# Kernel optimization log

Hardware: AMD Instinct MI355X
Metric: run time of the kernel (lower is better)

The kernel has to match this reference:

```python
import jax, jax.numpy as jnp
import numpy as np

N_NODES = 100000
N_EDGES = 800000
DIM = 300
N_GRAPHS = 64
ATOM_VOCAB = 41
WORD_VOCAB = 10000


def setup_inputs() -> dict:
    key = jax.random.key(0)
    ks = jax.random.split(key, 7)
    atoms = jax.random.randint(ks[0], (N_NODES,), 0, ATOM_VOCAB)
    words = jax.random.randint(ks[1], (N_NODES,), 0, WORD_VOCAB)
    x = jnp.stack([atoms, words], axis=-1)  # [N,2] int indices
    edge_index = jax.random.randint(ks[2], (2, N_EDGES), 0, N_NODES)
    batch = jnp.sort(jax.random.randint(ks[3], (N_NODES,), 0, N_GRAPHS))
    atom_table = jax.random.normal(ks[4], (ATOM_VOCAB, DIM), dtype=jnp.float32) * 0.02
    word_table = jax.random.normal(ks[5], (WORD_VOCAB, DIM), dtype=jnp.float32) * 0.02
    W = jax.random.normal(ks[6], (DIM, DIM), dtype=jnp.float32) / np.sqrt(DIM)
    b = jnp.zeros((DIM,), dtype=jnp.float32)
    return {"x": x, "edge_index": edge_index, "batch": batch,
            "atom_table": atom_table, "word_table": word_table,
            "W": W, "b": b, "num_hops": 3}


def reference(x, edge_index, batch, atom_table, word_table, W, b, num_hops):
    n = x.shape[0]
    # GCNConv: add self-loops, symmetric degree normalization
    loops = jnp.arange(n)
    src = jnp.concatenate([edge_index[0], loops])  # [E+N]
    dst = jnp.concatenate([edge_index[1], loops])
    deg = jax.ops.segment_sum(jnp.ones_like(dst, dtype=W.dtype), dst, num_segments=n)
    dinv = jnp.where(deg > 0, jax.lax.rsqrt(deg), 0.0)
    norm = dinv[src] * dinv[dst]  # [E+N]

    # embed_nodes: atom embedding + word embedding
    h = atom_table[x[:, 0]] + word_table[x[:, 1]]  # [N, D]

    # num_hops applications of the SAME GCNConv (shared W, b)
    for _ in range(num_hops):
        hw = h @ W  # [N, D]
        msg = hw[src] * norm[:, None]  # [E+N, D]
        h = jax.ops.segment_sum(msg, dst, num_segments=n) + b

    # global_mean_pool over batch assignment
    sums = jax.ops.segment_sum(h, batch, num_segments=N_GRAPHS)  # [G, D]
    cnt = jax.ops.segment_sum(jnp.ones((n,), h.dtype), batch, num_segments=N_GRAPHS)
    return sums / jnp.maximum(cnt, 1.0)[:, None]
```

## Files before the change

### kernel.cpp

```cpp
#include <hip/hip_runtime.h>
#include <hip/hip_fp16.h>

#define NG 64
#define NGRAPH_C 64
#define KPAD 10240

#define RSZ 12500
#define RSZP 6250
#define NC_MS 64

__device__ __forceinline__ unsigned f_as_u(float f) { union { float f; unsigned u; } c; c.f = f; return c.u; }
__device__ __forceinline__ float u_as_f(unsigned u) { union { unsigned u; float f; } c; c.u = u; return c.f; }

__device__ __forceinline__ int xcc_id() {
    unsigned x;
    asm volatile("s_getreg_b32 %0, hwreg(HW_REG_XCC_ID)" : "=s"(x));
    return (int)(x & 7u);
}

union H4 { uint2 u2; __half h[4]; };

__global__ __launch_bounds__(256) void k_mscount(const int* __restrict__ src, const int* __restrict__ dst,
                                                 unsigned* __restrict__ rep_in,
                                                 unsigned* __restrict__ rep_src,
                                                 int e, int n, int chunk, int npairs) {
    __shared__ unsigned hin[RSZP];
    __shared__ unsigned hsrc[RSZP];
    int c = blockIdx.x % NC_MS;
    int r = blockIdx.x / NC_MS;
    int base = r * RSZ;
    int t = threadIdx.x;
    for (int w = t; w < RSZP; w += 256) { hin[w] = 0u; hsrc[w] = 0u; }
    __syncthreads();
    int e0 = c * chunk, e1 = min(e, e0 + chunk);
    for (int i = e0 + t; i < e1; i += 256) {
        int s = src[i], d = dst[i];
        unsigned ud = (unsigned)(d - base);
        unsigned us = (unsigned)(s - base);
        if (ud < (unsigned)RSZ) atomicAdd(&hin[ud >> 1], 1u << ((ud & 1) * 16));
        if (us < (unsigned)RSZ) atomicAdd(&hsrc[us >> 1], 1u << ((us & 1) * 16));
    }
    __syncthreads();
    int lim = min(RSZ, n - base);
    if (lim <= 0) return;
    int plim = (lim + 1) >> 1;
    unsigned* gin  = rep_in  + (size_t)c * npairs + (base >> 1);
    unsigned* gsrc = rep_src + (size_t)c * npairs + (base >> 1);
    for (int w = t; w < plim; w += 256) { gin[w] = hin[w]; gsrc[w] = hsrc[w]; }
}

__global__ __launch_bounds__(256) void k_msreduce(const unsigned* __restrict__ rep_in,
                                                  unsigned* __restrict__ rep_src,
                                                  float* __restrict__ dinv,
                                                  unsigned* __restrict__ counts_src,
                                                  int n, int npairs) {
    int i2 = blockIdx.x * 256 + threadIdx.x;
    if (i2 >= npairs) return;
    unsigned slo = 0, shi = 0, rlo = 0, rhi = 0;
#pragma unroll 4
    for (int c = 0; c < NC_MS; ++c) {
        unsigned vi = rep_in[(size_t)c * npairs + i2];
        slo += vi & 0xFFFFu; shi += vi >> 16;
        unsigned vs = rep_src[(size_t)c * npairs + i2];
        rep_src[(size_t)c * npairs + i2] = rlo | (rhi << 16);
        rlo += vs & 0xFFFFu; rhi += vs >> 16;
    }
    int i = i2 * 2;
    dinv[i] = rsqrtf((float)(slo + 1u));
    counts_src[i] = rlo;
    if (i + 1 < n) {
        dinv[i + 1] = rsqrtf((float)(shi + 1u));
        counts_src[i + 1] = rhi;
    }
}

__global__ __launch_bounds__(256) void k_blocksum(const unsigned* __restrict__ counts,
                                                  unsigned* __restrict__ partials, int n) {
    __shared__ unsigned s[256];
    int base = blockIdx.x * 1024;
    unsigned sum = 0;
    for (int j = threadIdx.x; j < 1024; j += 256) {
        int i = base + j;
        sum += (i < n) ? counts[i] : 0u;
    }
    s[threadIdx.x] = sum;
    __syncthreads();
    for (int off = 128; off > 0; off >>= 1) {
        if (threadIdx.x < (unsigned)off) s[threadIdx.x] += s[threadIdx.x + off];
        __syncthreads();
    }
    if (threadIdx.x == 0) partials[blockIdx.x] = s[0];
}

__global__ __launch_bounds__(128) void k_scanpartials(unsigned* __restrict__ partials, int nb) {
    __shared__ unsigned s[128];
    int t = threadIdx.x;
    s[t] = (t < nb) ? partials[t] : 0u;
    __syncthreads();
    if (t == 0) {
        unsigned run = 0;
        for (int i = 0; i < nb; ++i) { unsigned v = s[i]; s[i] = run; run += v; }
    }
    __syncthreads();
    if (t < nb) partials[t] = s[t];
}

__global__ __launch_bounds__(256) void k_scanblock(const unsigned* __restrict__ counts,
                                                   const unsigned* __restrict__ partials,
                                                   unsigned* __restrict__ row_start, int n) {
    __shared__ unsigned s[256];
    int base = blockIdx.x * 1024;
    int t = threadIdx.x;
    unsigned v[4];
    unsigned tsum = 0;
#pragma unroll
    for (int j = 0; j < 4; ++j) {
        int i = base + t * 4 + j;
        v[j] = (i < n) ? counts[i] : 0u;
        tsum += v[j];
    }
    s[t] = tsum;
    __syncthreads();
    for (int off = 1; off < 256; off <<= 1) {
        unsigned x = (t >= off) ? s[t - off] : 0u;
        __syncthreads();
        s[t] += x;
        __syncthreads();
    }
    unsigned excl = (t > 0 ? s[t - 1] : 0u) + partials[blockIdx.x];
#pragma unroll
    for (int j = 0; j < 4; ++j) {
        int i = base + t * 4 + j;
        if (i < n) {
            row_start[i] = excl;
            excl += v[j];
            if (i == n - 1) row_start[n] = excl;
        }
    }
}

__global__ __launch_bounds__(256) void k_msfill(const int* __restrict__ src, const int* __restrict__ dst,
                                                const int* __restrict__ batch,
                                                const unsigned* __restrict__ row_start,
                                                const unsigned* __restrict__ pref,
                                                const float* __restrict__ dinv,
                                                uint2* __restrict__ euv,
                                                int e, int n, int chunk, int npairs) {
    __shared__ unsigned cur[RSZP];
    int c = blockIdx.x % NC_MS;
    int r = blockIdx.x / NC_MS;
    int base = r * RSZ;
    int t = threadIdx.x;
    for (int w = t; w < RSZP; w += 256) cur[w] = 0u;
    __syncthreads();
    int e0 = c * chunk, e1 = min(e, e0 + chunk);
    const unsigned* prefc = pref + (size_t)c * npairs;
    for (int i = e0 + t; i < e1; i += 256) {
        int s = src[i];
        unsigned us = (unsigned)(s - base);
        if (us < (unsigned)RSZ) {
            int d = dst[i];
            unsigned sh = (us & 1) * 16;
            unsigned old = atomicAdd(&cur[us >> 1], 1u << sh);
            unsigned slot = (old >> sh) & 0xFFFFu;
            unsigned p16 = (prefc[(unsigned)s >> 1] >> ((s & 1) * 16)) & 0xFFFFu;
            unsigned pos = row_start[s] + p16 + slot;
            uint2 pv;
            pv.x = (unsigned)d | ((unsigned)batch[d] << 17);
            pv.y = f_as_u(dinv[s] * dinv[d]);
            euv[pos] = pv;
        }
    }
}

__global__ __launch_bounds__(128) void k_gstart(const int* __restrict__ batch,
                                                int* __restrict__ gstart, int n, int ngraph) {
    int g = threadIdx.x;
    if (g > ngraph) return;
    if (g == ngraph) { gstart[g] = n; return; }
    int lo = 0, hi = n;
    while (lo < hi) {
        int mid = (lo + hi) >> 1;
        if (batch[mid] < g) lo = mid + 1; else hi = mid;
    }
    gstart[g] = lo;
}

__global__ __launch_bounds__(256) void k_y1(const int* __restrict__ batch,
                                            const float* __restrict__ dinv,
                                            const unsigned* __restrict__ row_start,
                                            const uint2* __restrict__ euv,
                                            __half* __restrict__ Y1, int n) {
    int idx = blockIdx.x * 256 + threadIdx.x;
    if (idx >= n * 16) return;
    int j = idx >> 4;
    int c4 = idx & 15;
    int cb = c4 * 4;
    float a0 = 0.f, a1 = 0.f, a2 = 0.f, a3 = 0.f;
    {
        int bj = batch[j];
        float dj = dinv[j];
        float sn = dj * dj;
        a0 += (bj == cb + 0) ? sn : 0.f;
        a1 += (bj == cb + 1) ? sn : 0.f;
        a2 += (bj == cb + 2) ? sn : 0.f;
        a3 += (bj == cb + 3) ? sn : 0.f;
    }
    unsigned e0 = row_start[j], e1 = row_start[j + 1];
    for (unsigned e = e0; e < e1; ++e) {
        uint2 p = euv[e];
        int bd = (int)(p.x >> 17);
        float v = u_as_f(p.y);
        a0 += (bd == cb + 0) ? v : 0.f;
        a1 += (bd == cb + 1) ? v : 0.f;
        a2 += (bd == cb + 2) ? v : 0.f;
        a3 += (bd == cb + 3) ? v : 0.f;
    }
    H4 o;
    o.h[0] = __float2half(a0); o.h[1] = __float2half(a1);
    o.h[2] = __float2half(a2); o.h[3] = __float2half(a3);
    *(uint2*)&Y1[(size_t)j * NG + cb] = o.u2;
}

__global__ __launch_bounds__(256) void k_yprop(const __half* __restrict__ Yin,
                                               const float* __restrict__ dinv,
                                               const unsigned* __restrict__ row_start,
                                               const uint2* __restrict__ euv,
                                               __half* __restrict__ Yout, int n) {
    int idx = blockIdx.x * 256 + threadIdx.x;
    if (idx >= n * 16) return;
    int j = idx >> 4;
    int c4 = idx & 15;
    int cb = c4 * 4;
    float dj = dinv[j];
    float sn = dj * dj;
    H4 s; s.u2 = *(const uint2*)&Yin[(size_t)j * NG + cb];
    float a0 = sn * __half2float(s.h[0]);
    float a1 = sn * __half2float(s.h[1]);
    float a2 = sn * __half2float(s.h[2]);
    float a3 = sn * __half2float(s.h[3]);
    unsigned e0 = row_start[j], e1 = row_start[j + 1];
    unsigned e = e0;
    for (; e + 2 <= e1; e += 2) {
        uint2 p0 = euv[e], p1 = euv[e + 1];
        float v0 = u_as_f(p0.y), v1 = u_as_f(p1.y);
        H4 m0; m0.u2 = *(const uint2*)&Yin[(size_t)(p0.x & 0x1FFFFu) * NG + cb];
        H4 m1; m1.u2 = *(const uint2*)&Yin[(size_t)(p1.x & 0x1FFFFu) * NG + cb];
        a0 += v0 * __half2float(m0.h[0]) + v1 * __half2float(m1.h[0]);
        a1 += v0 * __half2float(m0.h[1]) + v1 * __half2float(m1.h[1]);
        a2 += v0 * __half2float(m0.h[2]) + v1 * __half2float(m1.h[2]);
        a3 += v0 * __half2float(m0.h[3]) + v1 * __half2float(m1.h[3]);
    }
    if (e < e1) {
        uint2 p0 = euv[e];
        float v0 = u_as_f(p0.y);
        H4 m0; m0.u2 = *(const uint2*)&Yin[(size_t)(p0.x & 0x1FFFFu) * NG + cb];
        a0 += v0 * __half2float(m0.h[0]);
        a1 += v0 * __half2float(m0.h[1]);
        a2 += v0 * __half2float(m0.h[2]);
        a3 += v0 * __half2float(m0.h[3]);
    }
    H4 o;
    o.h[0] = __float2half(a0); o.h[1] = __float2half(a1);
    o.h[2] = __float2half(a2); o.h[3] = __float2half(a3);
    *(uint2*)&Yout[(size_t)j * NG + cb] = o.u2;
}

__global__ __launch_bounds__(256) void k_colsumh(const __half* __restrict__ Y,
                                                 float* __restrict__ su8, int n) {
    __shared__ float red[16][NG];
    int t = threadIdx.x;
    int cg = t & 15;
    int sr = t >> 4;
    float a0 = 0.f, a1 = 0.f, a2 = 0.f, a3 = 0.f;
    int stride = gridDim.x * 16;
    for (int j = blockIdx.x * 16 + sr; j < n; j += stride) {
        H4 v; v.u2 = *(const uint2*)&Y[(size_t)j * NG + cg * 4];
        a0 += __half2float(v.h[0]);
        a1 += __half2float(v.h[1]);
        a2 += __half2float(v.h[2]);
        a3 += __half2float(v.h[3]);
    }
    red[sr][cg * 4 + 0] = a0;
    red[sr][cg * 4 + 1] = a1;
    red[sr][cg * 4 + 2] = a2;
    red[sr][cg * 4 + 3] = a3;
    __syncthreads();
    if (t < NG) {
        float s = 0.f;
#pragma unroll
        for (int q = 0; q < 16; ++q) s += red[q][t];
        int r = xcc_id();
        __hip_atomic_fetch_add(&su8[r * NG + t], s,
                               __ATOMIC_RELAXED, __HIP_MEMORY_SCOPE_WORKGROUP);
    }
}

__global__ __launch_bounds__(256) void k_bucket(const __half* __restrict__ Y3,
                                                const int* __restrict__ x,
                                                float* __restrict__ tw,
                                                float* __restrict__ ta, int n) {
    __shared__ float lta[41 * NG];
    int t = threadIdx.x;
    for (int i = t; i < 41 * NG; i += 256) lta[i] = 0.f;
    __syncthreads();
    int g = t & 63;
    int s = t >> 6;
    for (int base = blockIdx.x * 4; base < n; base += gridDim.x * 4) {
        int j = base + s;
        if (j < n) {
            float y = __half2float(Y3[(size_t)j * NG + g]);
            int w = x[2 * j + 1];
            int a = x[2 * j];
            atomicAdd(&tw[(size_t)w * NG + g], y);
            atomicAdd(&lta[a * NG + g], y);
        }
    }
    __syncthreads();
    for (int i = t; i < 41 * NG; i += 256) atomicAdd(&ta[i], lta[i]);
}

__global__ __launch_bounds__(256) void k_wgemm2(const float* __restrict__ T,
                                                const float* __restrict__ Tab,
                                                float* __restrict__ G0) {
    __shared__ float Asm[32 * 64];
    __shared__ float Bsm[32 * 64];
    const int t = threadIdx.x;
    const int tg = t >> 4;
    const int tc = t & 15;
    const int c0 = blockIdx.x * 64;
    const int kb = blockIdx.y * 256;

    float acc[4][4] = {};

    for (int sub = 0; sub < 8; ++sub) {
        int kbase = kb + sub * 32;
#pragma unroll
        for (int r2 = 0; r2 < 2; ++r2) {
            int idx4 = r2 * 256 + t;
            int k = idx4 >> 4, g4 = idx4 & 15;
            float4 v = *(const float4*)&T[(size_t)(kbase + k) * 64 + g4 * 4];
            *(float4*)&Asm[k * 64 + g4 * 4] = v;
        }
#pragma unroll
        for (int r2 = 0; r2 < 2; ++r2) {
            int idx4 = r2 * 256 + t;
            int k = idx4 >> 4, c4i = idx4 & 15;
            int gk = kbase + k;
            int cb2 = c0 + c4i * 4;
            float4 v;
            if (gk < 10000 && cb2 + 3 < 300) {
                v = *(const float4*)&Tab[(size_t)gk * 300 + cb2];
            } else {
                float tmp[4];
#pragma unroll
                for (int q = 0; q < 4; ++q)
                    tmp[q] = (gk < 10000 && cb2 + q < 300) ? Tab[(size_t)gk * 300 + cb2 + q] : 0.f;
                v.x = tmp[0]; v.y = tmp[1]; v.z = tmp[2]; v.w = tmp[3];
            }
            *(float4*)&Bsm[k * 64 + c4i * 4] = v;
        }
        __syncthreads();
#pragma unroll 8
        for (int k = 0; k < 32; ++k) {
            float4 a4 = *(const float4*)&Asm[k * 64 + tg * 4];
            float4 b4 = *(const float4*)&Bsm[k * 64 + tc * 4];
            float a[4] = {a4.x, a4.y, a4.z, a4.w};
            float b[4] = {b4.x, b4.y, b4.z, b4.w};
#pragma unroll
            for (int i = 0; i < 4; ++i)
#pragma unroll
                for (int jj = 0; jj < 4; ++jj) acc[i][jj] += a[i] * b[jj];
        }
        __syncthreads();
    }

#pragma unroll
    for (int i = 0; i < 4; ++i) {
        int g = tg * 4 + i;
#pragma unroll
        for (int jj = 0; jj < 4; ++jj) {
            int c = c0 + tc * 4 + jj;
            if (c < 300) atomicAdd(&G0[g * 300 + c], acc[i][jj]);
        }
    }
}

__global__ __launch_bounds__(256) void k_agemm(const float* __restrict__ T,
                                               const float* __restrict__ Tab,
                                               float* __restrict__ G0) {
    int j = blockIdx.x * 256 + threadIdx.x;
    if (j >= NG * 300) return;
    int g = j / 300, c = j - g * 300;
    float acc = 0.f;
#pragma unroll
    for (int k = 0; k < 41; ++k) acc += T[(size_t)k * NG + g] * Tab[(size_t)k * 300 + c];
    atomicAdd(&G0[j], acc);
}

__global__ __launch_bounds__(256) void k_smm(const float* __restrict__ A,
                                             const float* __restrict__ W,
                                             float* __restrict__ C) {
    int j = blockIdx.x * 256 + threadIdx.x;
    if (j >= NG * 300) return;
    int g = j / 300, c = j - g * 300;
    int k0 = blockIdx.y * 60;
    float acc = 0.f;
#pragma unroll 1
    for (int k = k0; k < k0 + 60; k += 4) {
        float a0 = A[g * 300 + k + 0], a1 = A[g * 300 + k + 1];
        float a2 = A[g * 300 + k + 2], a3 = A[g * 300 + k + 3];
        float w0 = W[(k + 0) * 300 + c], w1 = W[(k + 1) * 300 + c];
        float w2 = W[(k + 2) * 300 + c], w3 = W[(k + 3) * 300 + c];
        acc += a0 * w0 + a1 * w1 + a2 * w2 + a3 * w3;
    }
    atomicAdd(&C[j], acc);
}

__global__ __launch_bounds__(256) void k_vec(const float* __restrict__ vin,
                                             const float* __restrict__ W,
                                             float* __restrict__ r_out) {
    int c = blockIdx.x * 256 + threadIdx.x;
    if (c >= 300) return;
    int k0 = blockIdx.y * 75;
    float acc = 0.f;
    for (int k = k0; k < k0 + 75; ++k) acc += vin[k] * W[k * 300 + c];
    atomicAdd(&r_out[c], acc);
}

__global__ __launch_bounds__(256) void k_out(const float* __restrict__ T3,
                                             const float* __restrict__ su1,
                                             const float* __restrict__ su2,
                                             const int* __restrict__ gstart,
                                             const float* __restrict__ r1,
                                             const float* __restrict__ r2,
                                             const float* __restrict__ b,
                                             float* __restrict__ out) {
    int j = blockIdx.x * 256 + threadIdx.x;
    if (j >= NG * 300) return;
    int g = j / 300, c = j - g * 300;
    int cnt = gstart[g + 1] - gstart[g];
    float s1 = 0.f, s2 = 0.f;
#pragma unroll
    for (int r = 0; r < 8; ++r) {
        s1 += su1[r * NG + g];
        s2 += su2[r * NG + g];
    }
    float v = T3[j] + s2 * r2[c] + s1 * r1[c] + (float)cnt * b[c];
    out[j] = v / (float)(cnt > 0 ? cnt : 1);
}

extern "C" void kernel_launch(void* const* d_in, const int* in_sizes, int n_in,
                              void* d_out, int out_size, void* d_ws, size_t ws_size,
                              hipStream_t stream) {
    const int*   x     = (const int*)d_in[0];
    const int*   ei    = (const int*)d_in[1];
    const int*   batch = (const int*)d_in[2];
    const float* at    = (const float*)d_in[3];
    const float* wt    = (const float*)d_in[4];
    const float* W     = (const float*)d_in[5];
    const float* b     = (const float*)d_in[6];

    const int n = in_sizes[0] / 2;
    const int e = in_sizes[1] / 2;

    char* ws = (char*)d_ws;
    size_t off = 0;
    auto carve = [&](size_t bytes) {
        void* p = ws + off;
        off += (bytes + 255) & ~(size_t)255;
        return p;
    };
    __half*   Y1        = (__half*)carve((size_t)n * NG * 2);
    __half*   Y2        = (__half*)carve((size_t)n * NG * 2);
    __half*   Y3        = (__half*)carve((size_t)n * NG * 2);
    uint2*    euv       = (uint2*)carve((size_t)e * 8);
    float*    dinv      = (float*)carve((size_t)n * 4);
    unsigned* counts_src= (unsigned*)carve((size_t)n * 4);
    unsigned* row_start = (unsigned*)carve((size_t)(n + 1) * 4);
    unsigned* partials  = (unsigned*)carve(1024 * 4);
    int*      gstart    = (int*)carve(65 * 4);
    char*     zB0       = (char*)carve(0);
    float*    su1       = (float*)carve((size_t)8 * NG * 4);
    float*    su2       = (float*)carve((size_t)8 * NG * 4);
    float*    ta        = (float*)carve((size_t)41 * NG * 4);
    float*    tw        = (float*)carve((size_t)KPAD * NG * 4);
    float*    G0        = (float*)carve((size_t)NG * 300 * 4);
    float*    r1        = (float*)carve(300 * 4);
    float*    r2        = (float*)carve(300 * 4);
    float*    T1        = (float*)carve((size_t)NG * 300 * 4);
    float*    T2        = (float*)carve((size_t)NG * 300 * 4);
    float*    T3        = (float*)carve((size_t)NG * 300 * 4);
    char*     zB1       = (char*)carve(0);

    const int* src = ei;
    const int* dst = ei + e;

    unsigned* rep_in  = (unsigned*)Y1;
    unsigned* rep_src = (unsigned*)Y2;

    hipMemsetAsync(zB0, 0, (size_t)(zB1 - zB0), stream);

    const int npairs = (n + 1) / 2;
    const int NRng   = (n + RSZ - 1) / RSZ;
    const int chunk  = (e + NC_MS - 1) / NC_MS;

    k_mscount<<<NRng * NC_MS, 256, 0, stream>>>(src, dst, rep_in, rep_src, e, n, chunk, npairs);
    k_msreduce<<<(npairs + 255) / 256, 256, 0, stream>>>(rep_in, rep_src, dinv, counts_src, n, npairs);
    int NB = (n + 1023) / 1024;
    k_blocksum<<<NB, 256, 0, stream>>>(counts_src, partials, n);
    k_scanpartials<<<1, 128, 0, stream>>>(partials, NB);
    k_scanblock<<<NB, 256, 0, stream>>>(counts_src, partials, row_start, n);
    k_msfill<<<NRng * NC_MS, 256, 0, stream>>>(src, dst, batch, row_start, rep_src, dinv, euv, e, n, chunk, npairs);
    k_gstart<<<1, 128, 0, stream>>>(batch, gstart, n, NGRAPH_C);

    int yb = (n * 16 + 255) / 256;
    k_y1<<<yb, 256, 0, stream>>>(batch, dinv, row_start, euv, Y1, n);
    k_colsumh<<<512, 256, 0, stream>>>(Y1, su1, n);
    k_yprop<<<yb, 256, 0, stream>>>(Y1, dinv, row_start, euv, Y2, n);
    k_colsumh<<<512, 256, 0, stream>>>(Y2, su2, n);
    k_yprop<<<yb, 256, 0, stream>>>(Y2, dinv, row_start, euv, Y3, n);

    k_bucket<<<256, 256, 0, stream>>>(Y3, x, tw, ta, n);
    {
        dim3 gw(5, 40);
        k_wgemm2<<<gw, 256, 0, stream>>>(tw, wt, G0);
        k_agemm<<<(NG * 300 + 255) / 256, 256, 0, stream>>>(ta, at, G0);
    }

    {
        dim3 gs((NG * 300 + 255) / 256, 5);
        k_smm<<<gs, 256, 0, stream>>>(G0, W, T1);
        k_smm<<<gs, 256, 0, stream>>>(T1, W, T2);
        k_smm<<<gs, 256, 0, stream>>>(T2, W, T3);
        dim3 gv(2, 4);
        k_vec<<<gv, 256, 0, stream>>>(b, W, r1);
        k_vec<<<gv, 256, 0, stream>>>(r1, W, r2);
    }

    k_out<<<(NG * 300 + 255) / 256, 256, 0, stream>>>(T3, su1, su2, gstart, r1, r2, b, (float*)d_out);
}
```

Baseline: 367.0 us.

## Replace word-embedding atomic bucketing with counting-sort gather fused into per-block GEMM

Nodes are counting-sorted by word index up front, using a multi-split histogram, a scan and a fill. The old global float-atomic scatter into a 10000x64 table is then replaced by a per-word gather-sum, fused with a partial GEMM against the word table in each block. Per-block partial results are written to a scratch buffer that reuses Y1 and reduced in a separate kernel. The sort adds several small launches, and the fused GEMM holds a 75-float accumulator per thread, which raises register pressure.

Result: slower. 467.6 us (+27.4%).

```diff
diff --git a/kernel.cpp b/kernel.cpp
--- a/kernel.cpp
+++ b/kernel.cpp
@@ -3,11 +3,16 @@
 
 #define NG 64
 #define NGRAPH_C 64
-#define KPAD 10240
 
 #define RSZ 12500
 #define RSZP 6250
 #define NC_MS 64
+
+#define VOC 10000
+#define VOCP 5000
+#define NC_W 128
+#define WB 40
+#define NWB 250
 
 __device__ __forceinline__ unsigned f_as_u(float f) { union { float f; unsigned u; } c; c.f = f; return c.u; }
 __device__ __forceinline__ float u_as_f(unsigned u) { union { unsigned u; float f; } c; c.u = u; return c.f; }
@@ -170,6 +175,61 @@
             pv.y = f_as_u(dinv[s] * dinv[d]);
             euv[pos] = pv;
         }
+    }
+}
+
+__global__ __launch_bounds__(256) void k_wmscount(const int* __restrict__ x,
+                                                  unsigned* __restrict__ rep_w,
+                                                  int n, int chunk) {
+    __shared__ unsigned h[VOCP];
+    int c = blockIdx.x;
+    int t = threadIdx.x;
+    for (int w = t; w < VOCP; w += 256) h[w] = 0u;
+    __syncthreads();
+    int j0 = c * chunk, j1 = min(n, j0 + chunk);
+    for (int j = j0 + t; j < j1; j += 256) {
+        int w = x[2 * j + 1];
+        atomicAdd(&h[w >> 1], 1u << ((w & 1) * 16));
+    }
+    __syncthreads();
+    unsigned* g = rep_w + (size_t)c * VOCP;
+    for (int w = t; w < VOCP; w += 256) g[w] = h[w];
+}
+
+__global__ __launch_bounds__(256) void k_wmsreduce(unsigned* __restrict__ rep_w,
+                                                   unsigned* __restrict__ counts_w) {
+    int i2 = blockIdx.x * 256 + threadIdx.x;
+    if (i2 >= VOCP) return;
+    unsigned rlo = 0, rhi = 0;
+#pragma unroll 4
+    for (int c = 0; c < NC_W; ++c) {
+        unsigned v = rep_w[(size_t)c * VOCP + i2];
+        rep_w[(size_t)c * VOCP + i2] = rlo | (rhi << 16);
+        rlo += v & 0xFFFFu; rhi += v >> 16;
+    }
+    counts_w[2 * i2] = rlo;
+    counts_w[2 * i2 + 1] = rhi;
+}
+
+__global__ __launch_bounds__(256) void k_wmsfill(const int* __restrict__ x,
+                                                 const unsigned* __restrict__ wstart,
+                                                 const unsigned* __restrict__ pref,
+                                                 unsigned* __restrict__ sorted,
+                                                 int n, int chunk) {
+    __shared__ unsigned cur[VOCP];
+    int c = blockIdx.x;
+    int t = threadIdx.x;
+    for (int w = t; w < VOCP; w += 256) cur[w] = 0u;
+    __syncthreads();
+    int j0 = c * chunk, j1 = min(n, j0 + chunk);
+    const unsigned* prefc = pref + (size_t)c * VOCP;
+    for (int j = j0 + t; j < j1; j += 256) {
+        int w = x[2 * j + 1];
+        unsigned sh = (w & 1) * 16;
+        unsigned old = atomicAdd(&cur[w >> 1], 1u << sh);
+        unsigned slot = (old >> sh) & 0xFFFFu;
+        unsigned p16 = (prefc[w >> 1] >> sh) & 0xFFFFu;
+        sorted[wstart[w] + p16 + slot] = (unsigned)j;
     }
 }
 
@@ -296,94 +356,70 @@
     }
 }
 
-__global__ __launch_bounds__(256) void k_bucket(const __half* __restrict__ Y3,
-                                                const int* __restrict__ x,
-                                                float* __restrict__ tw,
-                                                float* __restrict__ ta, int n) {
+__global__ __launch_bounds__(256) void k_ta(const __half* __restrict__ Y3,
+                                            const int* __restrict__ x,
+                                            float* __restrict__ ta, int n) {
     __shared__ float lta[41 * NG];
     int t = threadIdx.x;
     for (int i = t; i < 41 * NG; i += 256) lta[i] = 0.f;
     __syncthreads();
     int g = t & 63;
-    int s = t >> 6;
-    for (int base = blockIdx.x * 4; base < n; base += gridDim.x * 4) {
-        int j = base + s;
-        if (j < n) {
-            float y = __half2float(Y3[(size_t)j * NG + g]);
-            int w = x[2 * j + 1];
-            int a = x[2 * j];
-            atomicAdd(&tw[(size_t)w * NG + g], y);
-            atomicAdd(&lta[a * NG + g], y);
+    int sv = t >> 6;
+    for (int j = blockIdx.x * 4 + sv; j < n; j += gridDim.x * 4) {
+        float y = __half2float(Y3[(size_t)j * NG + g]);
+        int a = x[2 * j];
+        atomicAdd(&lta[a * NG + g], y);
+    }
+    __syncthreads();
+    for (int i = t; i < 41 * NG; i += 256) atomicAdd(&ta[i], lta[i]);
+}
+
+__global__ __launch_bounds__(256) void k_wfused(const __half* __restrict__ Y3,
+                                                const unsigned* __restrict__ sorted,
+                                                const unsigned* __restrict__ wstart,
+                                                const float* __restrict__ wt,
+                                                float* __restrict__ Gpart) {
+    __shared__ float tl[WB * NG];
+    int b = blockIdx.x;
+    int w0 = b * WB;
+    int t = threadIdx.x;
+    int g = t & 63;
+    int wv = t >> 6;
+    for (int w = wv; w < WB; w += 4) {
+        unsigned i0 = wstart[w0 + w], i1 = wstart[w0 + w + 1];
+        float s = 0.f;
+        for (unsigned idx = i0; idx < i1; ++idx) {
+            unsigned j = sorted[idx];
+            s += __half2float(Y3[(size_t)j * NG + g]);
         }
-    }
-    __syncthreads();
-    for (int i = t; i < 41 * NG; i += 256) atomicAdd(&ta[i], lta[i]);
-}
-
-__global__ __launch_bounds__(256) void k_wgemm2(const float* __restrict__ T,
-                                                const float* __restrict__ Tab,
-                                                float* __restrict__ G0) {
-    __shared__ float Asm[32 * 64];
-    __shared__ float Bsm[32 * 64];
-    const int t = threadIdx.x;
-    const int tg = t >> 4;
-    const int tc = t & 15;
-    const int c0 = blockIdx.x * 64;
-    const int kb = blockIdx.y * 256;
-
-    float acc[4][4] = {};
-
-    for (int sub = 0; sub < 8; ++sub) {
-        int kbase = kb + sub * 32;
-#pragma unroll
-        for (int r2 = 0; r2 < 2; ++r2) {
-            int idx4 = r2 * 256 + t;
-            int k = idx4 >> 4, g4 = idx4 & 15;
-            float4 v = *(const float4*)&T[(size_t)(kbase + k) * 64 + g4 * 4];
-            *(float4*)&Asm[k * 64 + g4 * 4] = v;
-        }
-#pragma unroll
-        for (int r2 = 0; r2 < 2; ++r2) {
-            int idx4 = r2 * 256 + t;
-            int k = idx4 >> 4, c4i = idx4 & 15;
-            int gk = kbase + k;
-            int cb2 = c0 + c4i * 4;
-            float4 v;
-            if (gk < 10000 && cb2 + 3 < 300) {
-                v = *(const float4*)&Tab[(size_t)gk * 300 + cb2];
-            } else {
-                float tmp[4];
-#pragma unroll
-                for (int q = 0; q < 4; ++q)
-                    tmp[q] = (gk < 10000 && cb2 + q < 300) ? Tab[(size_t)gk * 300 + cb2 + q] : 0.f;
-                v.x = tmp[0]; v.y = tmp[1]; v.z = tmp[2]; v.w = tmp[3];
-            }
-            *(float4*)&Bsm[k * 64 + c4i * 4] = v;
-        }
-        __syncthreads();
-#pragma unroll 8
-        for (int k = 0; k < 32; ++k) {
-            float4 a4 = *(const float4*)&Asm[k * 64 + tg * 4];
-            float4 b4 = *(const float4*)&Bsm[k * 64 + tc * 4];
-            float a[4] = {a4.x, a4.y, a4.z, a4.w};
-            float b[4] = {b4.x, b4.y, b4.z, b4.w};
-#pragma unroll
-            for (int i = 0; i < 4; ++i)
-#pragma unroll
-                for (int jj = 0; jj < 4; ++jj) acc[i][jj] += a[i] * b[jj];
-        }
-        __syncthreads();
-    }
-
-#pragma unroll
-    for (int i = 0; i < 4; ++i) {
-        int g = tg * 4 + i;
-#pragma unroll
-        for (int jj = 0; jj < 4; ++jj) {
-            int c = c0 + tc * 4 + jj;
-            if (c < 300) atomicAdd(&G0[g * 300 + c], acc[i][jj]);
-        }
-    }
+        tl[w * NG + g] = s;
+    }
+    __syncthreads();
+    int qs = __builtin_amdgcn_readfirstlane(wv);
+    const float* wtb = wt + (size_t)w0 * 300 + qs * 75;
+    float acc[75];
+#pragma unroll
+    for (int i = 0; i < 75; ++i) acc[i] = 0.f;
+    for (int w = 0; w < WB; ++w) {
+        float tg = tl[w * NG + g];
+        const float* wr = wtb + w * 300;
+#pragma unroll
+        for (int i = 0; i < 75; ++i) acc[i] += tg * wr[i];
+    }
+    float* gp = Gpart + (size_t)b * (NG * 300) + g * 300 + qs * 75;
+#pragma unroll
+    for (int i = 0; i < 75; ++i) gp[i] = acc[i];
+}
+
+__global__ __launch_bounds__(256) void k_greduce(const float* __restrict__ Gpart,
+                                                 float* __restrict__ G0) {
+    int k = blockIdx.x * 256 + threadIdx.x;
+    if (k >= NG * 300) return;
+    int p0 = (NWB * blockIdx.y) / 4;
+    int p1 = (NWB * (blockIdx.y + 1)) / 4;
+    float s = 0.f;
+    for (int p = p0; p < p1; ++p) s += Gpart[(size_t)p * (NG * 300) + k];
+    atomicAdd(&G0[k], s);
 }
 
 __global__ __launch_bounds__(256) void k_agemm(const float* __restrict__ T,
@@ -480,11 +516,12 @@
     unsigned* row_start = (unsigned*)carve((size_t)(n + 1) * 4);
     unsigned* partials  = (unsigned*)carve(1024 * 4);
     int*      gstart    = (int*)carve(65 * 4);
+    unsigned* wstart    = (unsigned*)carve((size_t)(VOC + 1) * 4);
+    unsigned* sorted    = (unsigned*)carve((size_t)n * 4);
     char*     zB0       = (char*)carve(0);
     float*    su1       = (float*)carve((size_t)8 * NG * 4);
     float*    su2       = (float*)carve((size_t)8 * NG * 4);
     float*    ta        = (float*)carve((size_t)41 * NG * 4);
-    float*    tw        = (float*)carve((size_t)KPAD * NG * 4);
     float*    G0        = (float*)carve((size_t)NG * 300 * 4);
     float*    r1        = (float*)carve(300 * 4);
     float*    r2        = (float*)carve(300 * 4);
@@ -498,12 +535,15 @@
 
     unsigned* rep_in  = (unsigned*)Y1;
     unsigned* rep_src = (unsigned*)Y2;
+    unsigned* rep_w   = (unsigned*)Y3;
+    float*    Gpart   = (float*)Y1;
 
     hipMemsetAsync(zB0, 0, (size_t)(zB1 - zB0), stream);
 
     const int npairs = (n + 1) / 2;
     const int NRng   = (n + RSZ - 1) / RSZ;
     const int chunk  = (e + NC_MS - 1) / NC_MS;
+    const int wchunk = (n + NC_W - 1) / NC_W;
 
     k_mscount<<<NRng * NC_MS, 256, 0, stream>>>(src, dst, rep_in, rep_src, e, n, chunk, npairs);
     k_msreduce<<<(npairs + 255) / 256, 256, 0, stream>>>(rep_in, rep_src, dinv, counts_src, n, npairs);
@@ -514,6 +554,14 @@
     k_msfill<<<NRng * NC_MS, 256, 0, stream>>>(src, dst, batch, row_start, rep_src, dinv, euv, e, n, chunk, npairs);
     k_gstart<<<1, 128, 0, stream>>>(batch, gstart, n, NGRAPH_C);
 
+    k_wmscount<<<NC_W, 256, 0, stream>>>(x, rep_w, n, wchunk);
+    k_wmsreduce<<<(VOCP + 255) / 256, 256, 0, stream>>>(rep_w, counts_src);
+    int NBW = (VOC + 1023) / 1024;
+    k_blocksum<<<NBW, 256, 0, stream>>>(counts_src, partials, VOC);
+    k_scanpartials<<<1, 128, 0, stream>>>(partials, NBW);
+    k_scanblock<<<NBW, 256, 0, stream>>>(counts_src, partials, wstart, VOC);
+    k_wmsfill<<<NC_W, 256, 0, stream>>>(x, wstart, rep_w, sorted, n, wchunk);
+
     int yb = (n * 16 + 255) / 256;
     k_y1<<<yb, 256, 0, stream>>>(batch, dinv, row_start, euv, Y1, n);
     k_colsumh<<<512, 256, 0, stream>>>(Y1, su1, n);
@@ -521,12 +569,13 @@
     k_colsumh<<<512, 256, 0, stream>>>(Y2, su2, n);
     k_yprop<<<yb, 256, 0, stream>>>(Y2, dinv, row_start, euv, Y3, n);
 
-    k_bucket<<<256, 256, 0, stream>>>(Y3, x, tw, ta, n);
+    k_ta<<<128, 256, 0, stream>>>(Y3, x, ta, n);
+    k_wfused<<<NWB, 256, 0, stream>>>(Y3, sorted, wstart, wt, Gpart);
     {
-        dim3 gw(5, 40);
-        k_wgemm2<<<gw, 256, 0, stream>>>(tw, wt, G0);
-        k_agemm<<<(NG * 300 + 255) / 256, 256, 0, stream>>>(ta, at, G0);
-    }
+        dim3 gr((NG * 300 + 255) / 256, 4);
+        k_greduce<<<gr, 256, 0, stream>>>(Gpart, G0);
+    }
+    k_agemm<<<(NG * 300 + 255) / 256, 256, 0, stream>>>(ta, at, G0);
 
     {
         dim3 gs((NG * 300 + 255) / 256, 5);
```

## Bucket nodes by word index and use split-K partials instead of global atomics

Applied to the files above, without the earlier changes.

The old design scatter-added every node's Y3 row into the word table with global float atomics. The new code counting-sorts node indices by word id (count, scan, fill) and gathers per word with atomic-free sums. The word GEMM now splits K into smaller chunks and writes partial results into a scratch buffer that reuses Y1. A separate reduction kernel then folds those partials into G0. This adds several small kernel launches and extra scratch traffic in exchange for removing the contended atomics.

Result: no change. 372.3 us (+1.5%).

```diff
diff --git a/kernel.cpp b/kernel.cpp
--- a/kernel.cpp
+++ b/kernel.cpp
@@ -3,11 +3,15 @@
 
 #define NG 64
 #define NGRAPH_C 64
-#define KPAD 10240
 
 #define RSZ 12500
 #define RSZP 6250
 #define NC_MS 64
+
+#define VOC 10000
+#define KPAD 10240
+#define NKC 80
+#define WGK 128
 
 __device__ __forceinline__ unsigned f_as_u(float f) { union { float f; unsigned u; } c; c.f = f; return c.u; }
 __device__ __forceinline__ float u_as_f(unsigned u) { union { unsigned u; float f; } c; c.u = u; return c.f; }
@@ -171,6 +175,45 @@
             euv[pos] = pv;
         }
     }
+}
+
+__global__ __launch_bounds__(256) void k_wcount(const int* __restrict__ x,
+                                                unsigned* __restrict__ wcnt, int n) {
+    int j = blockIdx.x * 256 + threadIdx.x;
+    if (j >= n) return;
+    atomicAdd(&wcnt[x[2 * j + 1]], 1u);
+}
+
+__global__ __launch_bounds__(256) void k_wfill(const int* __restrict__ x,
+                                               const unsigned* __restrict__ wstart,
+                                               unsigned* __restrict__ wcur,
+                                               unsigned* __restrict__ sorted, int n) {
+    int j = blockIdx.x * 256 + threadIdx.x;
+    if (j >= n) return;
+    int w = x[2 * j + 1];
+    unsigned pos = wstart[w] + atomicAdd(&wcur[w], 1u);
+    sorted[pos] = (unsigned)j;
+}
+
+__global__ __launch_bounds__(256) void k_twfill(const __half* __restrict__ Y3,
+                                                const unsigned* __restrict__ sorted,
+                                                const unsigned* __restrict__ wstart,
+                                                float* __restrict__ tw) {
+    int w = blockIdx.x * 4 + (threadIdx.x >> 6);
+    int g = threadIdx.x & 63;
+    if (w >= VOC) return;
+    unsigned i0 = wstart[w], i1 = wstart[w + 1];
+    float s = 0.f;
+    unsigned i = i0;
+    for (; i + 2 <= i1; i += 2) {
+        unsigned j0 = sorted[i], j1 = sorted[i + 1];
+        s += __half2float(Y3[(size_t)j0 * NG + g]) + __half2float(Y3[(size_t)j1 * NG + g]);
+    }
+    if (i < i1) {
+        unsigned j0 = sorted[i];
+        s += __half2float(Y3[(size_t)j0 * NG + g]);
+    }
+    tw[(size_t)w * NG + g] = s;
 }
 
 __global__ __launch_bounds__(128) void k_gstart(const int* __restrict__ batch,
@@ -296,25 +339,19 @@
     }
 }
 
-__global__ __launch_bounds__(256) void k_bucket(const __half* __restrict__ Y3,
-                                                const int* __restrict__ x,
-                                                float* __restrict__ tw,
-                                                float* __restrict__ ta, int n) {
+__global__ __launch_bounds__(256) void k_ta(const __half* __restrict__ Y3,
+                                            const int* __restrict__ x,
+                                            float* __restrict__ ta, int n) {
     __shared__ float lta[41 * NG];
     int t = threadIdx.x;
     for (int i = t; i < 41 * NG; i += 256) lta[i] = 0.f;
     __syncthreads();
     int g = t & 63;
-    int s = t >> 6;
-    for (int base = blockIdx.x * 4; base < n; base += gridDim.x * 4) {
-        int j = base + s;
-        if (j < n) {
-            float y = __half2float(Y3[(size_t)j * NG + g]);
-            int w = x[2 * j + 1];
-            int a = x[2 * j];
-            atomicAdd(&tw[(size_t)w * NG + g], y);
-            atomicAdd(&lta[a * NG + g], y);
-        }
+    int sv = t >> 6;
+    for (int j = blockIdx.x * 4 + sv; j < n; j += gridDim.x * 4) {
+        float y = __half2float(Y3[(size_t)j * NG + g]);
+        int a = x[2 * j];
+        atomicAdd(&lta[a * NG + g], y);
     }
     __syncthreads();
     for (int i = t; i < 41 * NG; i += 256) atomicAdd(&ta[i], lta[i]);
@@ -322,18 +359,18 @@
 
 __global__ __launch_bounds__(256) void k_wgemm2(const float* __restrict__ T,
                                                 const float* __restrict__ Tab,
-                                                float* __restrict__ G0) {
+                                                float* __restrict__ Gpart) {
     __shared__ float Asm[32 * 64];
     __shared__ float Bsm[32 * 64];
     const int t = threadIdx.x;
     const int tg = t >> 4;
     const int tc = t & 15;
     const int c0 = blockIdx.x * 64;
-    const int kb = blockIdx.y * 256;
+    const int kb = blockIdx.y * WGK;
 
     float acc[4][4] = {};
 
-    for (int sub = 0; sub < 8; ++sub) {
+    for (int sub = 0; sub < WGK / 32; ++sub) {
         int kbase = kb + sub * 32;
 #pragma unroll
         for (int r2 = 0; r2 < 2; ++r2) {
@@ -349,13 +386,13 @@
             int gk = kbase + k;
             int cb2 = c0 + c4i * 4;
             float4 v;
-            if (gk < 10000 && cb2 + 3 < 300) {
+            if (gk < VOC && cb2 + 3 < 300) {
                 v = *(const float4*)&Tab[(size_t)gk * 300 + cb2];
             } else {
                 float tmp[4];
 #pragma unroll
                 for (int q = 0; q < 4; ++q)
-                    tmp[q] = (gk < 10000 && cb2 + q < 300) ? Tab[(size_t)gk * 300 + cb2 + q] : 0.f;
+                    tmp[q] = (gk < VOC && cb2 + q < 300) ? Tab[(size_t)gk * 300 + cb2 + q] : 0.f;
                 v.x = tmp[0]; v.y = tmp[1]; v.z = tmp[2]; v.w = tmp[3];
             }
             *(float4*)&Bsm[k * 64 + c4i * 4] = v;
@@ -375,15 +412,27 @@
         __syncthreads();
     }
 
+    float* gp = Gpart + (size_t)blockIdx.y * (NG * 300);
 #pragma unroll
     for (int i = 0; i < 4; ++i) {
         int g = tg * 4 + i;
 #pragma unroll
         for (int jj = 0; jj < 4; ++jj) {
             int c = c0 + tc * 4 + jj;
-            if (c < 300) atomicAdd(&G0[g * 300 + c], acc[i][jj]);
+            if (c < 300) gp[g * 300 + c] = acc[i][jj];
         }
     }
+}
+
+__global__ __launch_bounds__(256) void k_greduce(const float* __restrict__ Gpart,
+                                                 float* __restrict__ G0) {
+    int k = blockIdx.x * 256 + threadIdx.x;
+    if (k >= NG * 300) return;
+    int p0 = blockIdx.y * (NKC / 8);
+    int p1 = p0 + (NKC / 8);
+    float s = 0.f;
+    for (int p = p0; p < p1; ++p) s += Gpart[(size_t)p * (NG * 300) + k];
+    atomicAdd(&G0[k], s);
 }
 
 __global__ __launch_bounds__(256) void k_agemm(const float* __restrict__ T,
@@ -480,6 +529,8 @@
     unsigned* row_start = (unsigned*)carve((size_t)(n + 1) * 4);
     unsigned* partials  = (unsigned*)carve(1024 * 4);
     int*      gstart    = (int*)carve(65 * 4);
+    unsigned* wstart    = (unsigned*)carve((size_t)(VOC + 1) * 4);
+    unsigned* sorted    = (unsigned*)carve((size_t)n * 4);
     char*     zB0       = (char*)carve(0);
     float*    su1       = (float*)carve((size_t)8 * NG * 4);
     float*    su2       = (float*)carve((size_t)8 * NG * 4);
@@ -491,6 +542,8 @@
     float*    T1        = (float*)carve((size_t)NG * 300 * 4);
     float*    T2        = (float*)carve((size_t)NG * 300 * 4);
     float*    T3        = (float*)carve((size_t)NG * 300 * 4);
+    unsigned* wcnt      = (unsigned*)carve((size_t)VOC * 4);
+    unsigned* wcur      = (unsigned*)carve((size_t)VOC * 4);
     char*     zB1       = (char*)carve(0);
 
     const int* src = ei;
@@ -498,6 +551,7 @@
 
     unsigned* rep_in  = (unsigned*)Y1;
     unsigned* rep_src = (unsigned*)Y2;
+    float*    Gpart   = (float*)Y1;
 
     hipMemsetAsync(zB0, 0, (size_t)(zB1 - zB0), stream);
 
@@ -514,6 +568,14 @@
     k_msfill<<<NRng * NC_MS, 256, 0, stream>>>(src, dst, batch, row_start, rep_src, dinv, euv, e, n, chunk, npairs);
     k_gstart<<<1, 128, 0, stream>>>(batch, gstart, n, NGRAPH_C);
 
+    int nb256 = (n + 255) / 256;
+    k_wcount<<<nb256, 256, 0, stream>>>(x, wcnt, n);
+    int NBW = (VOC + 1023) / 1024;
+    k_blocksum<<<NBW, 256, 0, stream>>>(wcnt, partials, VOC);
+    k_scanpartials<<<1, 128, 0, stream>>>(partials, NBW);
+    k_scanblock<<<NBW, 256, 0, stream>>>(wcnt, partials, wstart, VOC);
+    k_wfill<<<nb256, 256, 0, stream>>>(x, wstart, wcur, sorted, n);
+
     int yb = (n * 16 + 255) / 256;
     k_y1<<<yb, 256, 0, stream>>>(batch, dinv, row_start, euv, Y1, n);
     k_colsumh<<<512, 256, 0, stream>>>(Y1, su1, n);
@@ -521,12 +583,15 @@
     k_colsumh<<<512, 256, 0, stream>>>(Y2, su2, n);
     k_yprop<<<yb, 256, 0, stream>>>(Y2, dinv, row_start, euv, Y3, n);
 
-    k_bucket<<<256, 256, 0, stream>>>(Y3, x, tw, ta, n);
+    k_ta<<<256, 256, 0, stream>>>(Y3, x, ta, n);
+    k_twfill<<<(VOC + 3) / 4, 256, 0, stream>>>(Y3, sorted, wstart, tw);
     {
-        dim3 gw(5, 40);
-        k_wgemm2<<<gw, 256, 0, stream>>>(tw, wt, G0);
-        k_agemm<<<(NG * 300 + 255) / 256, 256, 0, stream>>>(ta, at, G0);
-    }
+        dim3 gw(5, NKC);
+        k_wgemm2<<<gw, 256, 0, stream>>>(tw, wt, Gpart);
+        dim3 gr((NG * 300 + 255) / 256, 8);
+        k_greduce<<<gr, 256, 0, stream>>>(Gpart, G0);
+    }
+    k_agemm<<<(NG * 300 + 255) / 256, 256, 0, stream>>>(ta, at, G0);
 
     {
         dim3 gs((NG * 300 + 255) / 256, 5);
```
